# Kernel tuning notes

Measured on AMD Instinct MI355X. Metric: run time of the kernel, lower is better.

Reference implementation:

```python
import jax, jax.numpy as jnp
import numpy as np

RADIUS = 0.1
LOOP = False


def _radius_adj(pos, r, loop):
    # pairwise squared distances via GEMM: ||a-b||^2 = ||a||^2 + ||b||^2 - 2 a.b
    sq = jnp.sum(pos * pos, axis=-1)                      # [N]
    d2 = sq[:, None] + sq[None, :] - 2.0 * (pos @ pos.T)  # [N, N]
    adj = d2 <= r * r
    if not loop:
        n = pos.shape[0]
        adj = adj & ~jnp.eye(n, dtype=bool)
    return adj


def setup_inputs() -> dict:
    key = jax.random.key(0)
    k1, _ = jax.random.split(key)
    N = 8192
    domain = jnp.ones((3,), dtype=jnp.float32)
    positions = jax.random.uniform(k1, (N, 3), dtype=jnp.float32) * domain
    return {"positions": positions, "domain": domain}


def reference(positions, domain):
    # Pass 1: unshifted radius graph.
    adj = _radius_adj(positions, RADIUS, LOOP)
    # Passes 2-4: shift by factor*domain, wrap back into the box, re-run
    # radius graph; torch.unique dedup of concatenated edge lists is exactly
    # the boolean OR of adjacencies.
    for factor in (0.25, 0.5, 0.75):
        shifted = jnp.remainder(positions + factor * domain, domain)
        adj = adj | _radius_adj(shifted, RADIUS, LOOP)
    return adj  # [N, N] bool adjacency == deduped edge_index
```

## Files before the change

kernel.cpp:

```cpp
#include <hip/hip_runtime.h>
#include <math.h>


typedef int iv4 __attribute__((ext_vector_type(4)));

__global__ __launch_bounds__(256) void gg_shift_kernel(
    const float* __restrict__ pos, const float* __restrict__ dom,
    float4* __restrict__ sp, int n)
{
#pragma clang fp contract(off)
    int i = blockIdx.x * blockDim.x + threadIdx.x;
    if (i >= n) return;
    float x = pos[3 * i + 0];
    float y = pos[3 * i + 1];
    float z = pos[3 * i + 2];
    float dx = dom[0], dy = dom[1], dz = dom[2];
#pragma unroll
    for (int k = 0; k < 4; ++k) {
        float sx, sy, sz;
        if (k == 0) {
            sx = x; sy = y; sz = z;
        } else {
            float f = 0.25f * (float)k;
            sx = fmodf(x + f * dx, dx);
            sy = fmodf(y + f * dy, dy);
            sz = fmodf(z + f * dz, dz);
        }
        float sq = ((sx * sx) + (sy * sy)) + (sz * sz);
        sp[(size_t)i * 4 + k] = make_float4(sx, sy, sz, sq);
    }
}

__global__ __launch_bounds__(256) void gg_adj_kernel(
    const float4* __restrict__ sp, const float* __restrict__ dom,
    int* __restrict__ out, int n)
{
    const int tid = threadIdx.x;
    const int tj = tid & 63;
    const int ti = tid >> 6;
    const int jbase = blockIdx.x * 256 + tj * 4;
    const int ibase = blockIdx.y * 32;
    const bool hasdiag = ((blockIdx.y >> 3) == blockIdx.x);

    const float dom0 = dom[0], dom1 = dom[1], dom2 = dom[2];

    __shared__ float4 si[32][4];
    for (int t = tid; t < 128; t += 256)
        si[t >> 2][t & 3] = sp[(size_t)(ibase + (t >> 2)) * 4 + (t & 3)];

    float4 jd0[4];
#pragma unroll
    for (int p = 0; p < 4; ++p)
        jd0[p] = sp[(size_t)(jbase + p) * 4 + 0];

    __syncthreads();

    const float RR  = 0.01f;
    const float EPS = 3e-5f;

    for (int iter = 0; iter < 8; ++iter) {
        const int irow = iter * 4 + ti;
        const int i = ibase + irow;
        const float4 i0 = si[irow][0];

        float d2m[4];
#pragma unroll
        for (int p = 0; p < 4; ++p) {
            const float dxv = i0.x - jd0[p].x;
            const float dyv = i0.y - jd0[p].y;
            const float dzv = i0.z - jd0[p].z;
            const float mx = fminf(fabsf(dxv), dom0 - fabsf(dxv));
            const float my = fminf(fabsf(dyv), dom1 - fabsf(dyv));
            const float mz = fminf(fabsf(dzv), dom2 - fabsf(dzv));
            d2m[p] = mx * mx + my * my + mz * mz;
        }

        bool b0 = d2m[0] <= RR, b1 = d2m[1] <= RR,
             b2 = d2m[2] <= RR, b3 = d2m[3] <= RR;

        const bool band = (fabsf(d2m[0] - RR) <= EPS) |
                          (fabsf(d2m[1] - RR) <= EPS) |
                          (fabsf(d2m[2] - RR) <= EPS) |
                          (fabsf(d2m[3] - RR) <= EPS);
        if (__builtin_expect(band, 0)) {
#pragma clang fp contract(off)
            bool bb[4] = {false, false, false, false};
#pragma unroll 1
            for (int k = 0; k < 4; ++k) {
                const float4 iv = si[irow][k];
#pragma unroll
                for (int p = 0; p < 4; ++p) {
                    const float4 jv = sp[(size_t)(jbase + p) * 4 + k];
                    float dot = __builtin_fmaf(iv.z, jv.z,
                                __builtin_fmaf(iv.y, jv.y, iv.x * jv.x));
                    float d2 = (iv.w + jv.w) - (2.0f * dot);
                    if (d2 <= RR) bb[p] = true;
                }
            }
            b0 = bb[0]; b1 = bb[1]; b2 = bb[2]; b3 = bb[3];
        }

        iv4 res;
        res.x = b0 ? 1 : 0;
        res.y = b1 ? 1 : 0;
        res.z = b2 ? 1 : 0;
        res.w = b3 ? 1 : 0;
        if (hasdiag) {
            if (i == jbase + 0) res.x = 0;
            if (i == jbase + 1) res.y = 0;
            if (i == jbase + 2) res.z = 0;
            if (i == jbase + 3) res.w = 0;
        }
        __builtin_nontemporal_store(
            res, reinterpret_cast<iv4*>(&out[(size_t)i * n + jbase]));
    }
}

extern "C" void kernel_launch(void* const* d_in, const int* in_sizes, int n_in,
                              void* d_out, int out_size, void* d_ws, size_t ws_size,
                              hipStream_t stream) {
    const float* pos = (const float*)d_in[0];
    const float* dom = (const float*)d_in[1];
    const int n = in_sizes[0] / 3;

    float4* sp = (float4*)d_ws;
    int* out = (int*)d_out;

    gg_shift_kernel<<<(n + 255) / 256, 256, 0, stream>>>(pos, dom, sp, n);

    dim3 grid(n / 256, n / 32);
    gg_adj_kernel<<<grid, 256, 0, stream>>>(sp, dom, out, n);
}
```

Before: 57.47 us.

## Fuse shift precompute into adjacency kernel and drop nontemporal stores

```diff
diff --git a/kernel.cpp b/kernel.cpp
--- a/kernel.cpp
+++ b/kernel.cpp
@@ -2,39 +2,11 @@
 #include <math.h>
 
 
-typedef int iv4 __attribute__((ext_vector_type(4)));
-
-__global__ __launch_bounds__(256) void gg_shift_kernel(
+__global__ __launch_bounds__(256) void gg_adj_kernel(
     const float* __restrict__ pos, const float* __restrict__ dom,
-    float4* __restrict__ sp, int n)
+    int* __restrict__ out, int n)
 {
 #pragma clang fp contract(off)
-    int i = blockIdx.x * blockDim.x + threadIdx.x;
-    if (i >= n) return;
-    float x = pos[3 * i + 0];
-    float y = pos[3 * i + 1];
-    float z = pos[3 * i + 2];
-    float dx = dom[0], dy = dom[1], dz = dom[2];
-#pragma unroll
-    for (int k = 0; k < 4; ++k) {
-        float sx, sy, sz;
-        if (k == 0) {
-            sx = x; sy = y; sz = z;
-        } else {
-            float f = 0.25f * (float)k;
-            sx = fmodf(x + f * dx, dx);
-            sy = fmodf(y + f * dy, dy);
-            sz = fmodf(z + f * dz, dz);
-        }
-        float sq = ((sx * sx) + (sy * sy)) + (sz * sz);
-        sp[(size_t)i * 4 + k] = make_float4(sx, sy, sz, sq);
-    }
-}
-
-__global__ __launch_bounds__(256) void gg_adj_kernel(
-    const float4* __restrict__ sp, const float* __restrict__ dom,
-    int* __restrict__ out, int n)
-{
     const int tid = threadIdx.x;
     const int tj = tid & 63;
     const int ti = tid >> 6;
@@ -45,13 +17,35 @@
     const float dom0 = dom[0], dom1 = dom[1], dom2 = dom[2];
 
     __shared__ float4 si[32][4];
-    for (int t = tid; t < 128; t += 256)
-        si[t >> 2][t & 3] = sp[(size_t)(ibase + (t >> 2)) * 4 + (t & 3)];
+    if (tid < 32) {
+        const int i = ibase + tid;
+        const float x = pos[3 * i + 0];
+        const float y = pos[3 * i + 1];
+        const float z = pos[3 * i + 2];
+#pragma unroll
+        for (int k = 0; k < 4; ++k) {
+            float sx, sy, sz;
+            if (k == 0) {
+                sx = x; sy = y; sz = z;
+            } else {
+                const float f = 0.25f * (float)k;
+                sx = fmodf(x + f * dom0, dom0);
+                sy = fmodf(y + f * dom1, dom1);
+                sz = fmodf(z + f * dom2, dom2);
+            }
+            const float sq = ((sx * sx) + (sy * sy)) + (sz * sz);
+            si[tid][k] = make_float4(sx, sy, sz, sq);
+        }
+    }
 
-    float4 jd0[4];
-#pragma unroll
-    for (int p = 0; p < 4; ++p)
-        jd0[p] = sp[(size_t)(jbase + p) * 4 + 0];
+    const float4 j0 = *(const float4*)&pos[3 * jbase + 0];
+    const float4 j1 = *(const float4*)&pos[3 * jbase + 4];
+    const float4 j2 = *(const float4*)&pos[3 * jbase + 8];
+    float jx[4], jy[4], jz[4];
+    jx[0] = j0.x; jy[0] = j0.y; jz[0] = j0.z;
+    jx[1] = j0.w; jy[1] = j1.x; jz[1] = j1.y;
+    jx[2] = j1.z; jy[2] = j1.w; jz[2] = j2.x;
+    jx[3] = j2.y; jy[3] = j2.z; jz[3] = j2.w;
 
     __syncthreads();
 
@@ -66,13 +60,13 @@
         float d2m[4];
 #pragma unroll
         for (int p = 0; p < 4; ++p) {
-            const float dxv = i0.x - jd0[p].x;
-            const float dyv = i0.y - jd0[p].y;
-            const float dzv = i0.z - jd0[p].z;
+            const float dxv = i0.x - jx[p];
+            const float dyv = i0.y - jy[p];
+            const float dzv = i0.z - jz[p];
             const float mx = fminf(fabsf(dxv), dom0 - fabsf(dxv));
             const float my = fminf(fabsf(dyv), dom1 - fabsf(dyv));
             const float mz = fminf(fabsf(dzv), dom2 - fabsf(dzv));
-            d2m[p] = mx * mx + my * my + mz * mz;
+            d2m[p] = ((mx * mx) + (my * my)) + (mz * mz);
         }
 
         bool b0 = d2m[0] <= RR, b1 = d2m[1] <= RR,
@@ -83,24 +77,32 @@
                           (fabsf(d2m[2] - RR) <= EPS) |
                           (fabsf(d2m[3] - RR) <= EPS);
         if (__builtin_expect(band, 0)) {
-#pragma clang fp contract(off)
             bool bb[4] = {false, false, false, false};
 #pragma unroll 1
             for (int k = 0; k < 4; ++k) {
                 const float4 iv = si[irow][k];
+                const float f = 0.25f * (float)k;
 #pragma unroll
                 for (int p = 0; p < 4; ++p) {
-                    const float4 jv = sp[(size_t)(jbase + p) * 4 + k];
-                    float dot = __builtin_fmaf(iv.z, jv.z,
-                                __builtin_fmaf(iv.y, jv.y, iv.x * jv.x));
-                    float d2 = (iv.w + jv.w) - (2.0f * dot);
+                    float sx, sy, sz;
+                    if (k == 0) {
+                        sx = jx[p]; sy = jy[p]; sz = jz[p];
+                    } else {
+                        sx = fmodf(jx[p] + f * dom0, dom0);
+                        sy = fmodf(jy[p] + f * dom1, dom1);
+                        sz = fmodf(jz[p] + f * dom2, dom2);
+                    }
+                    const float jsq = ((sx * sx) + (sy * sy)) + (sz * sz);
+                    float dot = __builtin_fmaf(iv.z, sz,
+                                __builtin_fmaf(iv.y, sy, iv.x * sx));
+                    float d2 = (iv.w + jsq) - (2.0f * dot);
                     if (d2 <= RR) bb[p] = true;
                 }
             }
             b0 = bb[0]; b1 = bb[1]; b2 = bb[2]; b3 = bb[3];
         }
 
-        iv4 res;
+        int4 res;
         res.x = b0 ? 1 : 0;
         res.y = b1 ? 1 : 0;
         res.z = b2 ? 1 : 0;
@@ -111,8 +113,7 @@
             if (i == jbase + 2) res.z = 0;
             if (i == jbase + 3) res.w = 0;
         }
-        __builtin_nontemporal_store(
-            res, reinterpret_cast<iv4*>(&out[(size_t)i * n + jbase]));
+        *reinterpret_cast<int4*>(&out[(size_t)i * n + jbase]) = res;
     }
 }
 
@@ -123,11 +124,8 @@
     const float* dom = (const float*)d_in[1];
     const int n = in_sizes[0] / 3;
 
-    float4* sp = (float4*)d_ws;
     int* out = (int*)d_out;
 
-    gg_shift_kernel<<<(n + 255) / 256, 256, 0, stream>>>(pos, dom, sp, n);
-
     dim3 grid(n / 256, n / 32);
-    gg_adj_kernel<<<grid, 256, 0, stream>>>(sp, dom, out, n);
+    gg_adj_kernel<<<grid, 256, 0, stream>>>(pos, dom, out, n);
 }
```

Result: no change. 57.49 us (+0.0%).
